# Kernel optimization log

Hardware: AMD Instinct MI355X
Metric: run time of the kernel (lower is better)

The kernel has to match this reference:

```python
import jax, jax.numpy as jnp
import numpy as np

# ---- exact Hungarian (Jonker-Volgenant / e-maxx shortest augmenting path) ----

def _lsa(cost):
    """Square cost matrix [n,n] (numpy) -> col index assigned to each row (optimal)."""
    n = cost.shape[0]
    a = np.zeros((n + 1, n + 1), dtype=np.float64)
    a[1:, 1:] = cost
    u = np.zeros(n + 1)
    v = np.zeros(n + 1)
    p = np.zeros(n + 1, dtype=np.int64)   # p[j] = row matched to column j (1-indexed)
    way = np.zeros(n + 1, dtype=np.int64)
    for i in range(1, n + 1):
        p[0] = i
        j0 = 0
        minv = np.full(n + 1, np.inf)
        used = np.zeros(n + 1, dtype=bool)
        while True:
            used[j0] = True
            i0 = p[j0]
            cur = a[i0] - u[i0] - v
            better = (~used) & (cur < minv)
            minv[better] = cur[better]
            way[better] = j0
            masked = np.where(used, np.inf, minv)
            j1 = int(np.argmin(masked))
            delta = masked[j1]
            u[p[used]] += delta
            v[used] -= delta
            minv[~used] -= delta
            j0 = j1
            if p[j0] == 0:
                break
        while j0 != 0:
            j1 = way[j0]
            p[j0] = p[j1]
            j0 = j1
    col = np.zeros(n, dtype=np.int64)
    for j in range(1, n + 1):
        col[p[j] - 1] = j - 1
    return col


def _lsa_batch(costs):
    """costs [..., N, N] numpy -> assigned col per row [..., N]."""
    N = costs.shape[-1]
    flat = costs.reshape(-1, N, N)
    cols = np.stack([_lsa(c) for c in flat])
    return cols.reshape(costs.shape[:-1])


# ---- kernel pieces (same math as cdist_torch / material_distances) ----

def _pair_sqdist(v1, v2):
    g = jnp.einsum('pnd,bmd->pbnm', v1, v2)
    s1 = (v1 ** 2).sum(-1)
    s2 = (v2 ** 2).sum(-1)
    return jnp.abs(-2.0 * g + s1[:, None, :, None] + s2[None, :, None, :])


def _self_sqdist(v):
    # v [B,N,d] -> [B,N,N]; only diagonal pairs of Material_kernel(x,x) are needed
    g = jnp.einsum('bnd,bmd->bnm', v, v)
    s = (v ** 2).sum(-1)
    return jnp.abs(-2.0 * g + s[:, :, None] + s[:, None, :])


def _material_kernel(D2, cols):
    # sum_i exp(-D2[..., i, cols[..., i]]) / N  (Hungarian-matched similarity)
    sel = jnp.take_along_axis(D2, cols[..., None], axis=-1)[..., 0]
    return jnp.exp(-sel).sum(-1) / D2.shape[-1]


def setup_inputs():
    key = jax.random.key(0)
    ks = jax.random.split(key, 4)
    P, B, A, d = 64, 32, 40, 128
    x = jax.random.normal(ks[0], (B, A, d), jnp.float32)
    data_points = jax.random.normal(ks[1], (P, A, d), jnp.float32)
    gamma = jnp.full((1, d), -2.0, jnp.float32)  # matches __init__: ones(1,n_in)*-2
    M = jax.random.normal(ks[2], (P, P), jnp.float32)
    K = M @ M.T + P * jnp.eye(P, dtype=jnp.float32)
    L = jnp.linalg.cholesky(K).astype(jnp.float32)  # valid trained-state Cholesky buffer
    alpha = jax.random.normal(ks[3], (P,), jnp.float32)
    return {"x": x, "data_points": data_points, "gamma": gamma, "L": L, "alpha": alpha}


def reference(x, data_points, gamma, L, alpha):
    g = jnp.exp(gamma)                      # [1,d]
    v1 = data_points * g                    # [P,A,d]
    v2 = x * g                              # [B,A,d]
    D2 = _pair_sqdist(v1, v2)               # [P,B,A,A]
    cols = jnp.asarray(_lsa_batch(np.asarray(D2, np.float64)))
    K_xnew = _material_kernel(D2, cols)     # [P,B]
    Linv = jnp.linalg.inv(L)
    v = Linv @ K_xnew                       # [P,B]
    mean = jnp.einsum('in,i->n', K_xnew, alpha)
    Ds = _self_sqdist(v2)                   # [B,A,A] (diagonal of K(x,x) only)
    cols_s = jnp.asarray(_lsa_batch(np.asarray(Ds, np.float64)))
    kxx = _material_kernel(Ds, cols_s)      # [B]
    var = kxx - jnp.einsum('in,in->n', v, v)
    return mean, var
```

## Files before the change

kernel.cpp:

```cpp
#include <hip/hip_runtime.h>
#include <math.h>

#define P_N 64
#define B_N 32
#define A_N 40
#define D_N 128

__device__ __forceinline__ int readlane_i(int v, int l) {
  return __builtin_amdgcn_readlane(v, l);
}
__device__ __forceinline__ float readlane_f(float v, int l) {
  return __int_as_float(__builtin_amdgcn_readlane(__float_as_int(v), l));
}
__device__ __forceinline__ unsigned ordf(float f) {
  unsigned b = __float_as_uint(f);
  return (b & 0x80000000u) ? ~b : (b | 0x80000000u);
}
__device__ __forceinline__ unsigned wave_min_u32(unsigned x) {
  unsigned t;
  t = (unsigned)__builtin_amdgcn_update_dpp((int)0xFFFFFFFFu, (int)x, 0x111, 0xF, 0xF, false);
  x = t < x ? t : x;
  t = (unsigned)__builtin_amdgcn_update_dpp((int)0xFFFFFFFFu, (int)x, 0x112, 0xF, 0xF, false);
  x = t < x ? t : x;
  t = (unsigned)__builtin_amdgcn_update_dpp((int)0xFFFFFFFFu, (int)x, 0x114, 0xF, 0xF, false);
  x = t < x ? t : x;
  t = (unsigned)__builtin_amdgcn_update_dpp((int)0xFFFFFFFFu, (int)x, 0x118, 0xF, 0xF, false);
  x = t < x ? t : x;
  t = (unsigned)__builtin_amdgcn_update_dpp((int)0xFFFFFFFFu, (int)x, 0x142, 0xA, 0xF, false);
  x = t < x ? t : x;
  t = (unsigned)__builtin_amdgcn_update_dpp((int)0xFFFFFFFFu, (int)x, 0x143, 0xC, 0xF, false);
  x = t < x ? t : x;
  return (unsigned)__builtin_amdgcn_readlane((int)x, 63);
}

__global__ __launch_bounds__(64) void hungarian_pair(
    const float* __restrict__ DP, const float* __restrict__ X,
    const float* __restrict__ G, float* __restrict__ out) {
  __shared__ float Cs[A_N * A_N];
  const int bid  = blockIdx.x;
  const int lane = threadIdx.x;
  const float* __restrict__ Abase = DP + (bid >> 5) * (A_N * D_N);
  const float* __restrict__ Bbase = X  + (bid & 31) * (A_N * D_N);

  if (lane < A_N) {
    const float* bp = Bbase + lane * D_N;
    for (int c = 0; c < 4; ++c) {
      float4 gg[8], bb[8];
      #pragma unroll
      for (int k = 0; k < 8; ++k) {
        float4 gr = ((const float4*)(G + c * 32))[k];
        gg[k] = make_float4(expf(gr.x), expf(gr.y), expf(gr.z), expf(gr.w));
        float4 br = ((const float4*)(bp + c * 32))[k];
        bb[k] = make_float4(br.x * gg[k].x, br.y * gg[k].y,
                            br.z * gg[k].z, br.w * gg[k].w);
      }
      for (int i = 0; i < A_N; ++i) {
        const float4* ap = (const float4*)(Abase + i * D_N + c * 32);
        float s = 0.f;
        #pragma unroll
        for (int k = 0; k < 8; ++k) {
          float4 a = ap[k];
          float dx = fmaf(a.x, gg[k].x, -bb[k].x); s = fmaf(dx, dx, s);
          float dy = fmaf(a.y, gg[k].y, -bb[k].y); s = fmaf(dy, dy, s);
          float dz = fmaf(a.z, gg[k].z, -bb[k].z); s = fmaf(dz, dz, s);
          float dw = fmaf(a.w, gg[k].w, -bb[k].w); s = fmaf(dw, dw, s);
        }
        if (c == 0) Cs[i * A_N + lane] = s;
        else        Cs[i * A_N + lane] += s;
      }
    }
  }
  __syncthreads();

  const int  cix     = (lane >= 1 && lane <= A_N) ? (lane - 1) : 0;
  const bool realcol = (lane >= 1 && lane <= A_N);

  float vpot = 0.f;
  int   amin = 0;
  if (realcol) {
    float mn = INFINITY; int mi = 0;
    for (int i = 0; i < A_N; ++i) {
      float c = Cs[i * A_N + cix];
      if (c < mn) { mn = c; mi = i; }
    }
    vpot = mn; amin = mi + 1;
  }

  unsigned long long rmask = 0ull;
  int p = 0, way = 0;
  for (int j = 1; j <= A_N; ++j) {
    int am = readlane_i(amin, j);
    if (!((rmask >> am) & 1ull)) {
      rmask |= 1ull << am;
      if (lane == j) p = am;
    }
  }

  float u = 0.f;

  for (int f = 1; f <= A_N; ++f) {
    if ((rmask >> f) & 1ull) continue;
    if (lane == 0) p = f;
    float mhat = INFINITY;
    float dsum = 0.f;
    float dent = 0.f, rent = 0.f;
    bool  used   = (lane == 0) || (lane > A_N);
    bool  intree = (lane == f);
    int   j0 = 0, i0 = f;
    for (int guard = 0; guard < 42; ++guard) {
      float Craw = Cs[(i0 - 1) * A_N + cix];
      float uc   = readlane_f(u, i0);
      float cand = Craw - uc - vpot + dsum;
      if (!used && cand < mhat) { mhat = cand; way = j0; }
      unsigned key = used ? 0xFFFFFFFFu
                   : ((ordf(mhat) & 0xFFFFF000u) | ((unsigned)p << 6) | (unsigned)lane);
      unsigned kmin = wave_min_u32(key);
      int j1 = (int)(kmin & 63u);
      int i1 = (int)((kmin >> 6) & 63u);
      dsum = readlane_f(mhat, j1);
      if (lane == j1) { used = true; dent = dsum; }
      j0 = j1;
      i0 = i1;
      if (i1 == 0) break;
      if (lane == i1) { intree = true; rent = dsum; }
    }
    if (used && realcol) vpot -= (dsum - dent);
    if (intree)          u    += (dsum - rent);
    while (j0 != 0) {
      int jn = readlane_i(way, j0);
      int pn = readlane_i(p, jn);
      if (lane == j0) p = pn;
      j0 = jn;
    }
  }

  float e = 0.f;
  if (realcol) e = expf(-Cs[(p - 1) * A_N + (lane - 1)]);
  #pragma unroll
  for (int off = 32; off; off >>= 1) e += __shfl_xor(e, off);
  if (lane == 0) out[bid] = e / 40.0f;
}

__global__ __launch_bounds__(64) void final_kernel(
    const float* __restrict__ Kx, const float* __restrict__ L,
    const float* __restrict__ alpha, float* __restrict__ out) {
  __shared__ float vl[P_N * B_N];
  int b = threadIdx.x;
  if (b >= B_N) return;
  float mean = 0.f;
  for (int p = 0; p < P_N; ++p) mean = fmaf(Kx[p * B_N + b], alpha[p], mean);
  out[b] = mean;
  float sumv2 = 0.f;
  for (int i = 0; i < P_N; ++i) {
    float s = Kx[i * B_N + b];
    for (int j = 0; j < i; ++j) s = fmaf(-L[i * P_N + j], vl[j * B_N + b], s);
    float vi = s / L[i * P_N + i];
    vl[i * B_N + b] = vi;
    sumv2 = fmaf(vi, vi, sumv2);
  }
  out[B_N + b] = 1.0f - sumv2;
}

extern "C" void kernel_launch(void* const* d_in, const int* in_sizes, int n_in,
                              void* d_out, int out_size, void* d_ws, size_t ws_size,
                              hipStream_t stream) {
  const float* x     = (const float*)d_in[0];
  const float* dp    = (const float*)d_in[1];
  const float* gamma = (const float*)d_in[2];
  const float* L     = (const float*)d_in[3];
  const float* alpha = (const float*)d_in[4];
  float* out = (float*)d_out;

  float* Kx = (float*)d_ws;

  hungarian_pair<<<P_N * B_N, 64, 0, stream>>>(dp, x, gamma, Kx);
  final_kernel<<<1, 64, 0, stream>>>(Kx, L, alpha, out);
}
```

Measured before the change: 149.7 us.

## Add row-reduction greedy init and branchless inner loop for Hungarian solver

Computes exp(gamma) once per block into LDS instead of per lane per chunk. Adds a second initialization pass that assigns each unmatched row to its cheapest free column using reduced costs, so fewer rows need the full augmenting-path search. The augmenting loop becomes branchless: used columns get an infinity offset instead of a conditional key, ordf is computed without a branch, and the per-lane key bits are hoisted out of the loop. The extra init pass adds wave reductions per row, and the infinity-masking must preserve exactness.

```diff
diff --git a/kernel.cpp b/kernel.cpp
--- a/kernel.cpp
+++ b/kernel.cpp
@@ -14,7 +14,7 @@
 }
 __device__ __forceinline__ unsigned ordf(float f) {
   unsigned b = __float_as_uint(f);
-  return (b & 0x80000000u) ? ~b : (b | 0x80000000u);
+  return b ^ (((unsigned)((int)b >> 31)) | 0x80000000u);
 }
 __device__ __forceinline__ unsigned wave_min_u32(unsigned x) {
   unsigned t;
@@ -37,10 +37,15 @@
     const float* __restrict__ DP, const float* __restrict__ X,
     const float* __restrict__ G, float* __restrict__ out) {
   __shared__ float Cs[A_N * A_N];
+  __shared__ float g_lds[D_N];
   const int bid  = blockIdx.x;
   const int lane = threadIdx.x;
   const float* __restrict__ Abase = DP + (bid >> 5) * (A_N * D_N);
   const float* __restrict__ Bbase = X  + (bid & 31) * (A_N * D_N);
+
+  g_lds[lane]      = expf(G[lane]);
+  g_lds[lane + 64] = expf(G[lane + 64]);
+  __syncthreads();
 
   if (lane < A_N) {
     const float* bp = Bbase + lane * D_N;
@@ -48,8 +53,7 @@
       float4 gg[8], bb[8];
       #pragma unroll
       for (int k = 0; k < 8; ++k) {
-        float4 gr = ((const float4*)(G + c * 32))[k];
-        gg[k] = make_float4(expf(gr.x), expf(gr.y), expf(gr.z), expf(gr.w));
+        gg[k] = ((const float4*)(g_lds + c * 32))[k];
         float4 br = ((const float4*)(bp + c * 32))[k];
         bb[k] = make_float4(br.x * gg[k].x, br.y * gg[k].y,
                             br.z * gg[k].z, br.w * gg[k].w);
@@ -98,31 +102,50 @@
 
   float u = 0.f;
 
+  for (int i = 1; i <= A_N; ++i) {
+    if ((rmask >> i) & 1ull) continue;
+    float r = realcol ? (Cs[(i - 1) * A_N + cix] - vpot) : INFINITY;
+    unsigned key = (ordf(r) & 0xFFFFFFC0u) | (unsigned)lane;
+    unsigned kmin = wave_min_u32(key);
+    int jm = (int)(kmin & 63u);
+    int pj = readlane_i(p, jm);
+    if (pj == 0) {
+      float rmin = readlane_f(r, jm);
+      if (lane == jm) p = i;
+      if (lane == i)  u = rmin;
+      rmask |= 1ull << i;
+    }
+  }
+
   for (int f = 1; f <= A_N; ++f) {
     if ((rmask >> f) & 1ull) continue;
     if (lane == 0) p = f;
     float mhat = INFINITY;
+    float excl = realcol ? 0.f : INFINITY;
     float dsum = 0.f;
     float dent = 0.f, rent = 0.f;
-    bool  used   = (lane == 0) || (lane > A_N);
+    bool  used   = !realcol;
     bool  intree = (lane == f);
     int   j0 = 0, i0 = f;
+    const unsigned plane_key = ((unsigned)p << 6) | (unsigned)lane;
     for (int guard = 0; guard < 42; ++guard) {
       float Craw = Cs[(i0 - 1) * A_N + cix];
       float uc   = readlane_f(u, i0);
-      float cand = Craw - uc - vpot + dsum;
-      if (!used && cand < mhat) { mhat = cand; way = j0; }
-      unsigned key = used ? 0xFFFFFFFFu
-                   : ((ordf(mhat) & 0xFFFFF000u) | ((unsigned)p << 6) | (unsigned)lane);
+      float off  = dsum - uc - vpot + excl;
+      float cand = Craw + off;
+      if (cand < mhat) way = j0;
+      mhat = fminf(mhat, cand);
+      unsigned key = (ordf(mhat) & 0xFFFFF000u) | plane_key;
       unsigned kmin = wave_min_u32(key);
       int j1 = (int)(kmin & 63u);
       int i1 = (int)((kmin >> 6) & 63u);
-      dsum = readlane_f(mhat, j1);
-      if (lane == j1) { used = true; dent = dsum; }
+      float dnew = readlane_f(mhat, j1);
+      if (lane == j1) { used = true; dent = dnew; excl = INFINITY; mhat = INFINITY; }
+      dsum = dnew;
       j0 = j1;
       i0 = i1;
       if (i1 == 0) break;
-      if (lane == i1) { intree = true; rent = dsum; }
+      if (lane == i1) { intree = true; rent = dnew; }
     }
     if (used && realcol) vpot -= (dsum - dent);
     if (intree)          u    += (dsum - rent);
```

After: 153.7 us. +2.7%, slower.
